# Performance work log

Measured on AMD Instinct MI355X. Metric: run time of the kernel, lower is better.

The kernel has to match this reference:

```python
import jax, jax.numpy as jnp
import numpy as np

B, S, I, E, NH, HID, L = 32, 512, 64, 128, 8, 1024, 4
HD = E // NH
TEMP = 0.05
EPS_BN = 1e-5
EPS_LN = 1e-5


def _pe(seq_len, d_model):
    # sinusoidal positional encoding, matches PositionalEncoding buffer pe[:seq_len, 0, :]
    pos = jnp.arange(seq_len, dtype=jnp.float32)[:, None]
    div = jnp.exp(jnp.arange(0, d_model, 2, dtype=jnp.float32) * (-np.log(10000.0) / d_model))
    pe = jnp.zeros((seq_len, d_model), jnp.float32)
    pe = pe.at[:, 0::2].set(jnp.sin(pos * div))
    pe = pe.at[:, 1::2].set(jnp.cos(pos * div))
    return pe


def _bn(x, g, b, axis):
    # eval-mode BatchNorm1d with running_mean=0, running_var=1 (affine scale+shift)
    sh = [1] * x.ndim
    sh[axis] = -1
    return x * (g / jnp.sqrt(1.0 + EPS_BN)).reshape(sh) + b.reshape(sh)


def _ln(x, g, b):
    m = jnp.mean(x, axis=-1, keepdims=True)
    v = jnp.var(x, axis=-1, keepdims=True)
    return (x - m) / jnp.sqrt(v + EPS_LN) * g + b


def _layer(h, Wqkv, bqkv, Wo, bo, g1, b1, g2, b2, W1, bf1, W2, bf2):
    # h: (S, B, E); post-LN torch TransformerEncoderLayer, relu FFN
    s, b = h.shape[0], h.shape[1]
    qkv = h @ Wqkv + bqkv                                  # (S, B, 3E)
    q, k, v = jnp.split(qkv, 3, axis=-1)
    sp = lambda t: t.reshape(s, b, NH, HD).transpose(1, 2, 0, 3)  # (B, NH, S, HD)
    q, k, v = sp(q), sp(k), sp(v)
    att = jax.nn.softmax(jnp.einsum('bhqd,bhkd->bhqk', q, k) * (1.0 / np.sqrt(HD)), axis=-1)
    o = jnp.einsum('bhqk,bhkd->bhqd', att, v).transpose(2, 0, 1, 3).reshape(s, b, E)
    h = _ln(h + o @ Wo + bo, g1, b1)
    ff = jax.nn.relu(h @ W1 + bf1) @ W2 + bf2
    h = _ln(h + ff, g2, b2)
    return h, att.mean(axis=1)  # attn averaged over heads: (B, S, S)


def setup_inputs() -> dict:
    key = jax.random.key(0)
    ks = iter(jax.random.split(key, 64))
    r = lambda *sh: jax.random.normal(next(ks), sh, jnp.float32) * 0.02
    return dict(
        x=jax.random.normal(next(ks), (B, S, I), jnp.float32),
        Wt=r(I, E), bt=r(E),
        bn1_g=jnp.ones(E), bn1_b=jnp.zeros(E),
        bn2_g=jnp.ones(E), bn2_b=jnp.zeros(E),
        Wqkv=r(L, E, 3 * E), bqkv=r(L, 3 * E), Wo=r(L, E, E), bo=r(L, E),
        ln1_g=jnp.ones((L, E)), ln1_b=jnp.zeros((L, E)),
        ln2_g=jnp.ones((L, E)), ln2_b=jnp.zeros((L, E)),
        W1=r(L, E, HID), b1=r(L, HID), W2=r(L, HID, E), b2=r(L, E),
        bn3_g=jnp.ones(E), bn3_b=jnp.zeros(E),
        Wd=r(E, I), bd=r(I), bn4_g=jnp.ones(I), bn4_b=jnp.zeros(I),
        Ws=r(S, HID), bs=r(HID), bn5_g=jnp.ones(HID), bn5_b=jnp.zeros(HID),
        Wtext=r(1024, HID), btext=r(HID), lnT_g=jnp.ones(HID), lnT_b=jnp.zeros(HID),
        sensor_emb=jax.random.normal(next(ks), (I, 1024), jnp.float32),
    )


def reference(x, Wt, bt, bn1_g, bn1_b, bn2_g, bn2_b,
              Wqkv, bqkv, Wo, bo, ln1_g, ln1_b, ln2_g, ln2_b,
              W1, b1, W2, b2, bn3_g, bn3_b,
              Wd, bd, bn4_g, bn4_b, Ws, bs, bn5_g, bn5_b,
              Wtext, btext, lnT_g, lnT_b, sensor_emb):
    # trunk_net: Linear -> BN(E) -> PE -> BN(E)
    h = x @ Wt + bt                                  # (B, S, E)
    h = _bn(h.transpose(0, 2, 1), bn1_g, bn1_b, 1)   # (B, E, S)
    h = h.transpose(2, 0, 1)                         # (S, B, E)
    h = h + _pe(h.shape[0], E)[:, None, :]
    h = _bn(h.transpose(1, 2, 0), bn2_g, bn2_b, 1)   # (B, E, S)
    h = h.transpose(2, 0, 1)                         # (S, B, E)
    for i in range(L):
        h, attn = _layer(h, Wqkv[i], bqkv[i], Wo[i], bo[i],
                         ln1_g[i], ln1_b[i], ln2_g[i], ln2_b[i],
                         W1[i], b1[i], W2[i], b2[i])
    h = _bn(h.transpose(1, 2, 0), bn3_g, bn3_b, 1)   # (B, E, S)
    # downsample_embedding_to_input_net
    d = jax.nn.relu(h.transpose(0, 2, 1) @ Wd + bd)  # (B, S, I)
    d = _bn(d.transpose(0, 2, 1), bn4_g, bn4_b, 1)   # (B, I, S)
    # sequence_representation_net
    imu = jax.nn.relu(d @ Ws + bs)                   # (B, I, HID)
    imu = _bn(imu, bn5_g, bn5_b, 2)
    # text_to_shared_net on sensor embeddings
    sens = _ln(jax.nn.relu(sensor_emb @ Wtext + btext), lnT_g, lnT_b)  # (I, HID)
    # fused pairwise cosine similarity (torch expands to (B,I,I,HID); we don't)
    imu_n = imu / jnp.maximum(jnp.linalg.norm(imu, axis=-1, keepdims=True), 1e-8)
    sens_n = sens / jnp.maximum(jnp.linalg.norm(sens, axis=-1, keepdims=True), 1e-8)
    return jnp.einsum('bih,jh->bij', imu_n, sens_n) / TEMP  # (B, I, I)
```

## Files before the change

### kernel.cpp

```cpp
#include <hip/hip_runtime.h>
#include <hip/hip_bf16.h>

#define B_   32
#define S_   512
#define I_   64
#define E_   128
#define NH_  8
#define HD_  16
#define HID_ 1024
#define L_   4
#define NTOK (B_*S_)

typedef __hip_bfloat16 bf16;
typedef __attribute__((ext_vector_type(8))) short bf16x8;
typedef __attribute__((ext_vector_type(4))) short bf16x4;
typedef __attribute__((ext_vector_type(4))) float f32x4;

__device__ __forceinline__ float b2f(bf16 v) { return __bfloat162float(v); }

template<bool F32>
__device__ __forceinline__ float ld(const void* p, size_t i) {
    if (F32) return ((const float*)p)[i];
    return b2f(((const bf16*)p)[i]);
}

__device__ __forceinline__ unsigned short f2bu(float f) {
    union { bf16 h; unsigned short u; } c; c.h = __float2bfloat16(f); return c.u;
}
__device__ __forceinline__ unsigned short b2u(bf16 h) {
    union { bf16 h; unsigned short u; } c; c.h = h; return c.u;
}
__device__ __forceinline__ float u2f(unsigned short u) {
    return __uint_as_float((unsigned int)u << 16);
}

__global__ void k_flag(const void* bn1g, int* flag) {
    if (threadIdx.x == 0) {
        const unsigned short* u = (const unsigned short*)bn1g;
        int zeros = 0;
        for (int i = 0; i < 32; ++i) zeros += (u[i] == 0);
        flag[0] = (zeros >= 8) ? 1 : 0;
    }
}

struct TrJobs {
    const void* in[7];
    bf16*       out[7];
    int R[7];
    int C[7];
    int start[8];
};

template<bool F32>
__device__ void tr_all_body(const TrJobs& j, float (*tile)[33])
{
    int bid = blockIdx.x;
    int job = 0;
#pragma unroll
    for (int t = 0; t < 6; ++t) if (bid >= j.start[t + 1]) job = t + 1;
    int local = bid - j.start[job];
    int R = j.R[job], C = j.C[job];
    int nx = C >> 5, ny = R >> 5;
    int per_z = nx * ny;
    int z = local / per_z;
    int rem = local - z * per_z;
    int cy = rem / nx, cx = rem - cy * nx;
    const void* in = j.in[job];
    bf16* out = j.out[job];

    size_t off = (size_t)z * R * C;
    int c0 = cx * 32, r0 = cy * 32;
    int tx = threadIdx.x;
    for (int i = threadIdx.y; i < 32; i += 8)
        tile[i][tx] = ld<F32>(in, off + (size_t)(r0 + i) * C + c0 + tx);
    __syncthreads();
    for (int i = threadIdx.y; i < 32; i += 8)
        out[off + (size_t)(c0 + i) * R + r0 + tx] = __float2bfloat16(tile[tx][i]);
}
__global__ __launch_bounds__(256) void k_tr_all(TrJobs j, const int* flag)
{
    __shared__ float tile[32][33];
    if (*flag) tr_all_body<true>(j, tile);
    else       tr_all_body<false>(j, tile);
}

template<bool F32>
__device__ void trunk_body(const void* x, const void* Wt, const void* bt,
                           const void* g1, const void* c1,
                           const void* g2, const void* c2, float* __restrict__ h,
                           float (*xs)[I_])
{
    const int TOK = 8;
    int t0 = blockIdx.x * TOK;
    int tid = threadIdx.x;
    for (int idx = tid; idx < TOK * I_; idx += 128) {
        int tt = idx >> 6, k = idx & 63;
        xs[tt][k] = ld<F32>(x, (size_t)(t0 + tt) * I_ + k);
    }
    __syncthreads();
    int e = tid;
    float acc[TOK];
    float bias = ld<F32>(bt, e);
#pragma unroll
    for (int tt = 0; tt < TOK; ++tt) acc[tt] = bias;
    for (int k = 0; k < I_; ++k) {
        float w = ld<F32>(Wt, k * E_ + e);
#pragma unroll
        for (int tt = 0; tt < TOK; ++tt) acc[tt] += xs[tt][k] * w;
    }
    float rs = rsqrtf(1.0f + 1e-5f);
    float a1 = ld<F32>(g1, e) * rs, d1 = ld<F32>(c1, e);
    float a2 = ld<F32>(g2, e) * rs, d2 = ld<F32>(c2, e);
    int p = e >> 1;
    float freq = __expf(-(float)p * 0.14391157f);
#pragma unroll
    for (int tt = 0; tt < TOK; ++tt) {
// ... 84 lines not shown
    const size_t base = (size_t)(b * S_) * 384 + hh * HD_;
    const float qs = 0.25f * 1.44269504f;

    for (int i = tid; i < S_ * 2; i += 512) {
        int s = i >> 1, hf = i & 1;
        uint4 v = *(const uint4*)(qkv + base + (size_t)s * 384 + 128 + hf * 8);
        unsigned int* w = (unsigned int*)&v;
#pragma unroll
        for (int j = 0; j < 4; ++j) {
            unsigned int lo = f2bu(u2f((unsigned short)(w[j] & 0xffff)) * qs);
            unsigned int hi = f2bu(u2f((unsigned short)(w[j] >> 16)) * qs);
            w[j] = lo | (hi << 16);
        }
        *(uint4*)&Ks[s * 16 + hf * 8] = v;
    }
    for (int i = tid; i < 256 * 2; i += 512) {
        int s = i >> 1, hf = i & 1;
        *(uint4*)&Qs[s * 16 + hf * 8] =
            *(const uint4*)(qkv + base + (size_t)(qh * 256 + s) * 384 + hf * 8);
    }
    {
        int s = tid;
        uint4 v0 = *(const uint4*)(qkv + base + (size_t)s * 384 + 256);
        uint4 v1 = *(const uint4*)(qkv + base + (size_t)s * 384 + 256 + 8);
        const unsigned short* u0 = (const unsigned short*)&v0;
        const unsigned short* u1 = (const unsigned short*)&v1;
#pragma unroll
        for (int dd = 0; dd < 8; ++dd) VT[dd * 520 + s] = u0[dd];
#pragma unroll
        for (int dd = 0; dd < 8; ++dd) VT[(8 + dd) * 520 + s] = u1[dd];
    }
    __syncthreads();

    int wv = tid >> 6, lane = tid & 63;
    int l15 = lane & 15, quad = lane >> 4;
    const f32x4 z4 = {0.f, 0.f, 0.f, 0.f};

    bf16x4 bq0 = *(const bf16x4*)&Qs[(wv * 32 + l15) * 16 + quad * 4];
    bf16x4 bq1 = *(const bf16x4*)&Qs[(wv * 32 + 16 + l15) * 16 + quad * 4];

    f32x4 O0 = z4, O1 = z4;
    float den0 = 0.f, den1 = 0.f;

#pragma unroll 2
    for (int kt = 0; kt < 32; ++kt) {
        bf16x4 ak = *(const bf16x4*)&Ks[(kt * 16 + l15) * 16 + quad * 4];
        bf16x4 av = *(const bf16x4*)&VT[l15 * 520 + kt * 16 + quad * 4];

        f32x4 s0 = __builtin_amdgcn_mfma_f32_16x16x16bf16_1k(ak, bq0, z4, 0, 0, 0);
        f32x4 s1 = __builtin_amdgcn_mfma_f32_16x16x16bf16_1k(ak, bq1, z4, 0, 0, 0);

        float p0[4], p1[4];
#pragma unroll
        for (int r = 0; r < 4; ++r) { p0[r] = exp2f(s0[r]); den0 += p0[r]; }
#pragma unroll
        for (int r = 0; r < 4; ++r) { p1[r] = exp2f(s1[r]); den1 += p1[r]; }

        bf16x4 pa0, pa1;
#pragma unroll
        for (int r = 0; r < 4; ++r) { pa0[r] = (short)f2bu(p0[r]); pa1[r] = (short)f2bu(p1[r]); }

        O0 = __builtin_amdgcn_mfma_f32_16x16x16bf16_1k(av, pa0, O0, 0, 0, 0);
        O1 = __builtin_amdgcn_mfma_f32_16x16x16bf16_1k(av, pa1, O1, 0, 0, 0);
    }

    den0 += __shfl_xor(den0, 16, 64);
    den0 += __shfl_xor(den0, 32, 64);
    den1 += __shfl_xor(den1, 16, 64);
    den1 += __shfl_xor(den1, 32, 64);
    float inv0 = 1.0f / den0;
    float inv1 = 1.0f / den1;

    int q0 = qh * 256 + wv * 32 + l15;
    bf16* out0 = qkv + (size_t)(b * S_ + q0) * 384 + hh * HD_ + quad * 4;
    bf16* out1 = out0 + (size_t)16 * 384;
    unsigned int a0 = (unsigned int)f2bu(O0[0] * inv0) | ((unsigned int)f2bu(O0[1] * inv0) << 16);
    unsigned int a1 = (unsigned int)f2bu(O0[2] * inv0) | ((unsigned int)f2bu(O0[3] * inv0) << 16);
    *(uint2*)out0 = (uint2){a0, a1};
    unsigned int c0 = (unsigned int)f2bu(O1[0] * inv1) | ((unsigned int)f2bu(O1[1] * inv1) << 16);
    unsigned int c1 = (unsigned int)f2bu(O1[2] * inv1) | ((unsigned int)f2bu(O1[3] * inv1) << 16);
    *(uint2*)out1 = (uint2){c0, c1};
}

#define FTOK 32
#define APAD 8
#define MPAD 8

template<bool F32>
__device__ void projffn_body(const bf16* __restrict__ qkv, const bf16* __restrict__ WoT,
                             const void* bo, size_t obo,
                             const void* g1, const void* be1,
                             const bf16* __restrict__ W1T, const void* b1, size_t ob1,
                             const bf16* __restrict__ W2T, const void* b2v, size_t ob2,
                             const void* g2, const void* be2, size_t oln,
                             float* __restrict__ h,
                             unsigned short (*A_s)[E_ + APAD],
                             unsigned short (*mid_s)[HID_ + MPAD],
                             float (*red)[32][2])
{
    int t0 = blockIdx.x * FTOK;
    int tid = threadIdx.x;
    int wv = tid >> 6, lane = tid & 63;
    int l15 = lane & 15, quad = lane >> 4;
    int c0 = wv * 32 + l15, c1 = c0 + 16;

    for (int i = tid; i < 32 * 16; i += 256) {
        int row = i >> 4, seg = i & 15;
        *(uint4*)&A_s[row][seg * 8] =
            *(const uint4*)&qkv[(size_t)(t0 + row) * 384 + seg * 8];
    }
    __syncthreads();

    bf16x8 af[2][4];
#pragma unroll
    for (int kt = 0; kt < 4; ++kt) {
        int k0 = kt * 32 + quad * 8;
        af[0][kt] = *(const bf16x8*)&A_s[l15][k0];
        af[1][kt] = *(const bf16x8*)&A_s[16 + l15][k0];
    }
    f32x4 acc[2][2];
#pragma unroll
    for (int a = 0; a < 2; ++a)
#pragma unroll
        for (int bn = 0; bn < 2; ++bn) acc[a][bn] = (f32x4){0.f, 0.f, 0.f, 0.f};
#pragma unroll
    for (int kt = 0; kt < 4; ++kt) {
        int k0 = kt * 32 + quad * 8;
        bf16x8 bb0 = *(const bf16x8*)&WoT[(size_t)c0 * E_ + k0];
        bf16x8 bb1 = *(const bf16x8*)&WoT[(size_t)c1 * E_ + k0];
        acc[0][0] = __builtin_amdgcn_mfma_f32_16x16x32_bf16(af[0][kt], bb0, acc[0][0], 0, 0, 0);
        acc[1][0] = __builtin_amdgcn_mfma_f32_16x16x32_bf16(af[1][kt], bb0, acc[1][0], 0, 0, 0);
        acc[0][1] = __builtin_amdgcn_mfma_f32_16x16x32_bf16(af[0][kt], bb1, acc[0][1], 0, 0, 0);
        acc[1][1] = __builtin_amdgcn_mfma_f32_16x16x32_bf16(af[1][kt], bb1, acc[1][1], 0, 0, 0);
    }

    float bo0 = ld<F32>(bo, obo + c0), bo1 = ld<F32>(bo, obo + c1);
    float val[2][2][4], s1[2][4], s2[2][4];
#pragma unroll
    for (int mt = 0; mt < 2; ++mt) {
#pragma unroll
        for (int r = 0; r < 4; ++r) {
            size_t row = (size_t)(t0 + mt * 16 + quad * 4 + r);
            float v0 = acc[mt][0][r] + bo0 + h[row * E_ + c0];
            float v1 = acc[mt][1][r] + bo1 + h[row * E_ + c1];
            val[mt][0][r] = v0; val[mt][1][r] = v1;
            s1[mt][r] = v0 + v1;
            s2[mt][r] = v0 * v0 + v1 * v1;
        }
    }
#pragma unroll
    for (int off = 1; off < 16; off <<= 1) {
#pragma unroll
        for (int mt = 0; mt < 2; ++mt)
#pragma unroll
            for (int r = 0; r < 4; ++r) {
                s1[mt][r] += __shfl_xor(s1[mt][r], off, 64);
                s2[mt][r] += __shfl_xor(s2[mt][r], off, 64);
            }
    }
    if (l15 == 0) {
#pragma unroll
        for (int mt = 0; mt < 2; ++mt)
#pragma unroll
            for (int r = 0; r < 4; ++r) {
                red[wv][mt * 16 + quad * 4 + r][0] = s1[mt][r];
                red[wv][mt * 16 + quad * 4 + r][1] = s2[mt][r];
            }
    }
    __syncthreads();

    float val1[2][2][4];
    {
        float g10 = ld<F32>(g1, oln + c0), g11 = ld<F32>(g1, oln + c1);
        float b10 = ld<F32>(be1, oln + c0), b11 = ld<F32>(be1, oln + c1);
#pragma unroll
        for (int mt = 0; mt < 2; ++mt) {
#pragma unroll
            for (int r = 0; r < 4; ++r) {
                int rw = mt * 16 + quad * 4 + r;
                float su = red[0][rw][0] + red[1][rw][0] + red[2][rw][0] + red[3][rw][0];
                float sq = red[0][rw][1] + red[1][rw][1] + red[2][rw][1] + red[3][rw][1];
                float mean = su * (1.0f / E_);
                float var = fmaxf(sq * (1.0f / E_) - mean * mean, 0.0f);
                float rstd = rsqrtf(var + 1e-5f);
                float h0 = (val[mt][0][r] - mean) * rstd * g10 + b10;
                float h1v = (val[mt][1][r] - mean) * rstd * g11 + b11;
                val1[mt][0][r] = h0; val1[mt][1][r] = h1v;
                A_s[rw][c0] = f2bu(h0);
                A_s[rw][c1] = f2bu(h1v);
            }
        }
    }
    __syncthreads();

    {
        bf16x8 af1[2][4];
#pragma unroll
        for (int kt = 0; kt < 4; ++kt) {
            int k0 = kt * 32 + quad * 8;
            af1[0][kt] = *(const bf16x8*)&A_s[l15][k0];
            af1[1][kt] = *(const bf16x8*)&A_s[16 + l15][k0];
        }
        for (int nt = 0; nt < 16; ++nt) {
            int col = wv * 256 + nt * 16 + l15;
            f32x4 acc0 = {0.f, 0.f, 0.f, 0.f}, acc1 = {0.f, 0.f, 0.f, 0.f};
#pragma unroll
            for (int kt = 0; kt < 4; ++kt) {
                bf16x8 bfr = *(const bf16x8*)&W1T[(size_t)col * E_ + kt * 32 + quad * 8];
                acc0 = __builtin_amdgcn_mfma_f32_16x16x32_bf16(af1[0][kt], bfr, acc0, 0, 0, 0);
                acc1 = __builtin_amdgcn_mfma_f32_16x16x32_bf16(af1[1][kt], bfr, acc1, 0, 0, 0);
            }
            float bias = ld<F32>(b1, ob1 + col);
#pragma unroll
            for (int r = 0; r < 4; ++r) {
                mid_s[quad * 4 + r][col]      = f2bu(fmaxf(acc0[r] + bias, 0.f));
                mid_s[16 + quad * 4 + r][col] = f2bu(fmaxf(acc1[r] + bias, 0.f));
            }
        }
    }
    __syncthreads();

    f32x4 acc2[2][2];
#pragma unroll
    for (int a = 0; a < 2; ++a)
#pragma unroll
        for (int bn = 0; bn < 2; ++bn) acc2[a][bn] = (f32x4){0.f, 0.f, 0.f, 0.f};
    for (int kt = 0; kt < 32; ++kt) {
        int k0 = kt * 32 + quad * 8;
        bf16x8 a0 = *(const bf16x8*)&mid_s[l15][k0];
        bf16x8 a1 = *(const bf16x8*)&mid_s[16 + l15][k0];
        bf16x8 bb0 = *(const bf16x8*)&W2T[(size_t)c0 * HID_ + k0];
        bf16x8 bb1 = *(const bf16x8*)&W2T[(size_t)c1 * HID_ + k0];
        acc2[0][0] = __builtin_amdgcn_mfma_f32_16x16x32_bf16(a0, bb0, acc2[0][0], 0, 0, 0);
        acc2[1][0] = __builtin_amdgcn_mfma_f32_16x16x32_bf16(a1, bb0, acc2[1][0], 0, 0, 0);
        acc2[0][1] = __builtin_amdgcn_mfma_f32_16x16x32_bf16(a0, bb1, acc2[0][1], 0, 0, 0);
        acc2[1][1] = __builtin_amdgcn_mfma_f32_16x16x32_bf16(a1, bb1, acc2[1][1], 0, 0, 0);
    }

    float b20 = ld<F32>(b2v, ob2 + c0), b21 = ld<F32>(b2v, ob2 + c1);
#pragma unroll
    for (int mt = 0; mt < 2; ++mt) {
#pragma unroll
        for (int r = 0; r < 4; ++r) {
            float v0 = acc2[mt][0][r] + b20 + val1[mt][0][r];
            float v1 = acc2[mt][1][r] + b21 + val1[mt][1][r];
            val[mt][0][r] = v0; val[mt][1][r] = v1;
            s1[mt][r] = v0 + v1;
            s2[mt][r] = v0 * v0 + v1 * v1;
        }
    }
#pragma unroll
    for (int off = 1; off < 16; off <<= 1) {
#pragma unroll
        for (int mt = 0; mt < 2; ++mt)
#pragma unroll
            for (int r = 0; r < 4; ++r) {
                s1[mt][r] += __shfl_xor(s1[mt][r], off, 64);
                s2[mt][r] += __shfl_xor(s2[mt][r], off, 64);
            }
    }
    if (l15 == 0) {
#pragma unroll
        for (int mt = 0; mt < 2; ++mt)
#pragma unroll
            for (int r = 0; r < 4; ++r) {
                red[wv][mt * 16 + quad * 4 + r][0] = s1[mt][r];
                red[wv][mt * 16 + quad * 4 + r][1] = s2[mt][r];
            }
    }
    __syncthreads();
    float g20 = ld<F32>(g2, oln + c0), g21 = ld<F32>(g2, oln + c1);
    float be20 = ld<F32>(be2, oln + c0), be21 = ld<F32>(be2, oln + c1);
#pragma unroll
    for (int mt = 0; mt < 2; ++mt) {
#pragma unroll
        for (int r = 0; r < 4; ++r) {
            int rw = mt * 16 + quad * 4 + r;
            float su = red[0][rw][0] + red[1][rw][0] + red[2][rw][0] + red[3][rw][0];
            float sq = red[0][rw][1] + red[1][rw][1] + red[2][rw][1] + red[3][rw][1];
            float mean = su * (1.0f / E_);
            float var = fmaxf(sq * (1.0f / E_) - mean * mean, 0.0f);
            float rstd = rsqrtf(var + 1e-5f);
            size_t row = (size_t)(t0 + rw);
            h[row * E_ + c0] = (val[mt][0][r] - mean) * rstd * g20 + be20;
            h[row * E_ + c1] = (val[mt][1][r] - mean) * rstd * g21 + be21;
        }
    }
}
__global__ __launch_bounds__(256) void k_projffn(
    const bf16* qkv, const bf16* WoT, const void* bo, size_t obo,
    const void* g1, const void* be1,
    const bf16* W1T, const void* b1, size_t ob1,
    const bf16* W2T, const void* b2v, size_t ob2,
    const void* g2, const void* be2, size_t oln, float* h, const int* flag)
{
    __shared__ unsigned short A_s[FTOK][E_ + APAD];
    __shared__ unsigned short mid_s[FTOK][HID_ + MPAD];
    __shared__ float red[4][32][2];
    if (*flag) projffn_body<true>(qkv, WoT, bo, obo, g1, be1, W1T, b1, ob1,
                                  W2T, b2v, ob2, g2, be2, oln, h, A_s, mid_s, red);
    else       projffn_body<false>(qkv, WoT, bo, obo, g1, be1, W1T, b1, ob1,
                                   W2T, b2v, ob2, g2, be2, oln, h, A_s, mid_s, red);
}

template<bool F32>
__device__ void downm_body(const float* __restrict__ h, const void* g3, const void* c3,
                           const bf16* __restrict__ WdT, const void* bd,
                           const void* g4, const void* c4, float* __restrict__ d,
                           unsigned short (*A_s)[136], float* g3s, float* c3s)
{
    int t0 = blockIdx.x * 32;
    int tid = threadIdx.x;
    if (tid < E_) {
        float rs = rsqrtf(1.0f + 1e-5f);
        g3s[tid] = ld<F32>(g3, tid) * rs;
        c3s[tid] = ld<F32>(c3, tid);
    }
    __syncthreads();
    for (int i = tid; i < 32 * E_; i += 256) {
        int row = i >> 7, col = i & 127;
        A_s[row][col] = f2bu(h[(size_t)(t0 + row) * E_ + col] * g3s[col] + c3s[col]);
    }
    __syncthreads();

    int wv = tid >> 6, lane = tid & 63;
    int l15 = lane & 15, quad = lane >> 4;
    int col = wv * 16 + l15;
    f32x4 acc0 = {0.f, 0.f, 0.f, 0.f}, acc1 = {0.f, 0.f, 0.f, 0.f};
#pragma unroll
    for (int kt = 0; kt < 4; ++kt) {
        int k0 = kt * 32 + quad * 8;
        bf16x8 a0 = *(const bf16x8*)&A_s[l15][k0];
        bf16x8 a1 = *(const bf16x8*)&A_s[16 + l15][k0];
        bf16x8 bb = *(const bf16x8*)&WdT[(size_t)col * E_ + k0];
        acc0 = __builtin_amdgcn_mfma_f32_16x16x32_bf16(a0, bb, acc0, 0, 0, 0);
        acc1 = __builtin_amdgcn_mfma_f32_16x16x32_bf16(a1, bb, acc1, 0, 0, 0);
    }
    float rs = rsqrtf(1.0f + 1e-5f);
    float bb = ld<F32>(bd, col);
    float a4 = ld<F32>(g4, col) * rs, d4 = ld<F32>(c4, col);
#pragma unroll
    for (int r = 0; r < 4; ++r) {
        d[(size_t)(t0 + quad * 4 + r) * I_ + col]      = fmaxf(acc0[r] + bb, 0.f) * a4 + d4;
        d[(size_t)(t0 + 16 + quad * 4 + r) * I_ + col] = fmaxf(acc1[r] + bb, 0.f) * a4 + d4;
    }
}
__global__ __launch_bounds__(256) void k_down(
    const float* h, const void* g3, const void* c3, const bf16* WdT, const void* bd,
    const void* g4, const void* c4, float* d, const int* flag)
{
    __shared__ unsigned short A_s[32][136];
    __shared__ float g3s[E_], c3s[E_];
    if (*flag) downm_body<true>(h, g3, c3, WdT, bd, g4, c4, d, A_s, g3s, c3s);
    else       downm_body<false>(h, g3, c3, WdT, bd, g4, c4, d, A_s, g3s, c3s);
}

template<bool F32>
__device__ void imum_body(const float* __restrict__ d, const bf16* __restrict__ WsT,
                          const void* bs, const void* g5, const void* c5,
                          float* __restrict__ imu, unsigned short (*A_s)[520])
{
    int b = blockIdx.x >> 3;
    int jc = blockIdx.x & 7;
    int tid = threadIdx.x;
    int wv = tid >> 6, lane = tid & 63;
    int l15 = lane & 15, quad = lane >> 4;

    for (int idx = tid; idx < I_ * S_; idx += 256) {
        int i = idx & 63, s = idx >> 6;
        A_s[i][s] = f2bu(d[((size_t)b * S_ + s) * I_ + i]);
    }
    __syncthreads();

    float rs = rsqrtf(1.0f + 1e-5f);
    int j0 = jc * 128 + wv * 32;
    for (int nt = 0; nt < 2; ++nt) {
        int j = j0 + nt * 16 + l15;
        f32x4 acc4[4];
#pragma unroll
        for (int mt = 0; mt < 4; ++mt) acc4[mt] = (f32x4){0.f, 0.f, 0.f, 0.f};
        for (int kt = 0; kt < 16; ++kt) {
            int k0 = kt * 32 + quad * 8;
            bf16x8 bfr = *(const bf16x8*)&WsT[(size_t)j * S_ + k0];
#pragma unroll
            for (int mt = 0; mt < 4; ++mt) {
// ... 184 lines not shown
extern "C" void kernel_launch(void* const* d_in, const int* in_sizes, int n_in,
                              void* d_out, int out_size, void* d_ws, size_t ws_size,
                              hipStream_t stream) {
    (void)in_sizes; (void)n_in; (void)out_size; (void)ws_size;
    const void* x      = d_in[0];
    const void* Wt     = d_in[1];
    const void* bt     = d_in[2];
    const void* bn1_g  = d_in[3];
    const void* bn1_b  = d_in[4];
    const void* bn2_g  = d_in[5];
    const void* bn2_b  = d_in[6];
    const void* Wqkv   = d_in[7];
    const void* bqkv   = d_in[8];
    const void* Wo     = d_in[9];
    const void* bo     = d_in[10];
    const void* ln1_g  = d_in[11];
    const void* ln1_b  = d_in[12];
    const void* ln2_g  = d_in[13];
    const void* ln2_b  = d_in[14];
    const void* W1     = d_in[15];
    const void* b1     = d_in[16];
    const void* W2     = d_in[17];
    const void* b2     = d_in[18];
    const void* bn3_g  = d_in[19];
    const void* bn3_b  = d_in[20];
    const void* Wd     = d_in[21];
    const void* bd     = d_in[22];
    const void* bn4_g  = d_in[23];
    const void* bn4_b  = d_in[24];
    const void* Wsr    = d_in[25];
    const void* bs     = d_in[26];
    const void* bn5_g  = d_in[27];
    const void* bn5_b  = d_in[28];
    const void* Wtext  = d_in[29];
    const void* btext  = d_in[30];
    const void* lnT_g  = d_in[31];
    const void* lnT_b  = d_in[32];
    const void* semb   = d_in[33];

    char* ws = (char*)d_ws;
    float* h    = (float*)(ws);
    bf16*  qkvb = (bf16*) (ws + ((size_t)8  << 20));
    float* dbuf = (float*)(ws + ((size_t)8  << 20));
    float* imu  = (float*)(ws + ((size_t)12 << 20));
    bf16*  wb   = (bf16*) (ws + ((size_t)20 << 20));
    bf16*  WqkvT = wb;
    bf16*  WoT   = wb + 196608;
    bf16*  W1T   = wb + 262144;
    bf16*  W2T   = wb + 786432;
    bf16*  WsT   = wb + 1310720;
    bf16*  sensb = wb + 1835008;
    bf16*  WdT   = wb + 1900544;
    float* sg    = (float*)(wb + 1908736);
    int*   flag  = (int*)  (ws + ((size_t)24 << 20));
    bf16*  WtxT  = (bf16*) (ws + ((size_t)25 << 20));

    k_flag<<<1, 64, 0, stream>>>(bn1_g, flag);

    {
        TrJobs tj;
        tj.in[0] = Wqkv;  tj.out[0] = WqkvT; tj.R[0] = 128;  tj.C[0] = 384;
        tj.in[1] = Wo;    tj.out[1] = WoT;   tj.R[1] = 128;  tj.C[1] = 128;
        tj.in[2] = W1;    tj.out[2] = W1T;   tj.R[2] = 128;  tj.C[2] = 1024;
        tj.in[3] = W2;    tj.out[3] = W2T;   tj.R[3] = 1024; tj.C[3] = 128;
        tj.in[4] = Wsr;   tj.out[4] = WsT;   tj.R[4] = 512;  tj.C[4] = 1024;
        tj.in[5] = Wd;    tj.out[5] = WdT;   tj.R[5] = 128;  tj.C[5] = 64;
        tj.in[6] = Wtext; tj.out[6] = WtxT;  tj.R[6] = 1024; tj.C[6] = 1024;
        const int st[8] = {0, 192, 256, 768, 1280, 1792, 1800, 2824};
        for (int i = 0; i < 8; ++i) tj.start[i] = st[i];
        k_tr_all<<<2824, dim3(32, 8), 0, stream>>>(tj, flag);
    }

    k_trunk<<<NTOK / 8, 128, 0, stream>>>(x, Wt, bt, bn1_g, bn1_b, bn2_g, bn2_b, h, flag);

    for (int l = 0; l < L_; ++l) {
        size_t obqkv = (size_t)l * 384;
        size_t obo   = (size_t)l * E_;
        size_t ob1   = (size_t)l * HID_;
        size_t ob2   = (size_t)l * E_;
        size_t oln   = (size_t)l * E_;
        k_qkv<<<NTOK / 32, 256, 0, stream>>>(h, WqkvT + (size_t)l * 49152,
                                             bqkv, obqkv, qkvb, flag);
        k_attn<<<B_ * NH_ * 2, 512, 0, stream>>>(qkvb);
        k_projffn<<<NTOK / 32, 256, 0, stream>>>(qkvb, WoT + (size_t)l * 16384, bo, obo,
                                                 ln1_g, ln1_b,
                                                 W1T + (size_t)l * 131072, b1, ob1,
                                                 W2T + (size_t)l * 131072, b2, ob2,
                                                 ln2_g, ln2_b, oln, h, flag);
    }

    k_down<<<NTOK / 32, 256, 0, stream>>>(h, bn3_g, bn3_b, WdT, bd, bn4_g, bn4_b, dbuf, flag);
    k_imu<<<B_ * 8, 256, 0, stream>>>(dbuf, WsT, bs, bn5_g, bn5_b, imu, flag);
    k_norm<<<B_ * I_, 256, 0, stream>>>(imu);
    k_sens_gemm<<<64, 256, 0, stream>>>(semb, WtxT, btext, sg, flag);
    k_sens_ln<<<I_, 256, 0, stream>>>(sg, lnT_g, lnT_b, sensb, flag);
    k_final<<<(B_ * I_) / 32, 256, 0, stream>>>(imu, sensb, d_out, flag);
}
```

Baseline: 520.8 us.

## Restructure fused proj+FFN kernel to register-resident per-wave token tiles without LDS

Rewrites the output-projection + LayerNorm + FFN + LayerNorm kernel so each wave owns 16 tokens and computes transposed MFMAs (weights as A operand, tokens as B) with 16x16x16 bf16 instructions. Activations stay in registers across the chain, so the LDS staging buffers, the cross-wave reductions and the block barriers go away, and the FFN hidden activation is consumed immediately per 16-column chunk instead of being written to a 32x1024 shared buffer. Grid halves to 64 tokens per block. The trade-off is more weight traffic per token from global/L2, since each wave reloads all weights, plus heavier register pressure.

```diff
diff --git a/kernel.cpp b/kernel.cpp
--- a/kernel.cpp
+++ b/kernel.cpp
@@ -32,6 +32,14 @@
 }
 __device__ __forceinline__ float u2f(unsigned short u) {
     return __uint_as_float((unsigned int)u << 16);
+}
+
+template<bool F32>
+__device__ __forceinline__ float4 ld4(const void* p, size_t i) {
+    if (F32) return *(const float4*)((const float*)p + i);
+    bf16x4 v = *(const bf16x4*)((const bf16*)p + i);
+    return make_float4(u2f((unsigned short)v[0]), u2f((unsigned short)v[1]),
+                       u2f((unsigned short)v[2]), u2f((unsigned short)v[3]));
 }
 
 __global__ void k_flag(const void* bn1g, int* flag) {
@@ -282,9 +290,7 @@
     *(uint2*)out1 = (uint2){c0, c1};
 }
 
-#define FTOK 32
-#define APAD 8
-#define MPAD 8
+#define MFMA16(A, Bv, C) __builtin_amdgcn_mfma_f32_16x16x16bf16_1k(A, Bv, C, 0, 0, 0)
 
 template<bool F32>
 __device__ void projffn_body(const bf16* __restrict__ qkv, const bf16* __restrict__ WoT,
@@ -293,197 +299,125 @@
                              const bf16* __restrict__ W1T, const void* b1, size_t ob1,
                              const bf16* __restrict__ W2T, const void* b2v, size_t ob2,
                              const void* g2, const void* be2, size_t oln,
-                             float* __restrict__ h,
-                             unsigned short (*A_s)[E_ + APAD],
-                             unsigned short (*mid_s)[HID_ + MPAD],
-                             float (*red)[32][2])
-{
-    int t0 = blockIdx.x * FTOK;
-    int tid = threadIdx.x;
-    int wv = tid >> 6, lane = tid & 63;
+                             float* __restrict__ h)
+{
+    int wv = threadIdx.x >> 6, lane = threadIdx.x & 63;
     int l15 = lane & 15, quad = lane >> 4;
-    int c0 = wv * 32 + l15, c1 = c0 + 16;
-
-    for (int i = tid; i < 32 * 16; i += 256) {
-        int row = i >> 4, seg = i & 15;
-        *(uint4*)&A_s[row][seg * 8] =
-            *(const uint4*)&qkv[(size_t)(t0 + row) * 384 + seg * 8];
-    }
-    __syncthreads();
-
-    bf16x8 af[2][4];
-#pragma unroll
-    for (int kt = 0; kt < 4; ++kt) {
-        int k0 = kt * 32 + quad * 8;
-        af[0][kt] = *(const bf16x8*)&A_s[l15][k0];
-        af[1][kt] = *(const bf16x8*)&A_s[16 + l15][k0];
-    }
-    f32x4 acc[2][2];
-#pragma unroll
-    for (int a = 0; a < 2; ++a)
-#pragma unroll
-        for (int bn = 0; bn < 2; ++bn) acc[a][bn] = (f32x4){0.f, 0.f, 0.f, 0.f};
-#pragma unroll
-    for (int kt = 0; kt < 4; ++kt) {
-        int k0 = kt * 32 + quad * 8;
-        bf16x8 bb0 = *(const bf16x8*)&WoT[(size_t)c0 * E_ + k0];
-        bf16x8 bb1 = *(const bf16x8*)&WoT[(size_t)c1 * E_ + k0];
-        acc[0][0] = __builtin_amdgcn_mfma_f32_16x16x32_bf16(af[0][kt], bb0, acc[0][0], 0, 0, 0);
-        acc[1][0] = __builtin_amdgcn_mfma_f32_16x16x32_bf16(af[1][kt], bb0, acc[1][0], 0, 0, 0);
-        acc[0][1] = __builtin_amdgcn_mfma_f32_16x16x32_bf16(af[0][kt], bb1, acc[0][1], 0, 0, 0);
-        acc[1][1] = __builtin_amdgcn_mfma_f32_16x16x32_bf16(af[1][kt], bb1, acc[1][1], 0, 0, 0);
-    }
-
-    float bo0 = ld<F32>(bo, obo + c0), bo1 = ld<F32>(bo, obo + c1);
-    float val[2][2][4], s1[2][4], s2[2][4];
-#pragma unroll
-    for (int mt = 0; mt < 2; ++mt) {
-#pragma unroll
-        for (int r = 0; r < 4; ++r) {
-            size_t row = (size_t)(t0 + mt * 16 + quad * 4 + r);
-            float v0 = acc[mt][0][r] + bo0 + h[row * E_ + c0];
-            float v1 = acc[mt][1][r] + bo1 + h[row * E_ + c1];
-            val[mt][0][r] = v0; val[mt][1][r] = v1;
-            s1[mt][r] = v0 + v1;
-            s2[mt][r] = v0 * v0 + v1 * v1;
-        }
-    }
-#pragma unroll
-    for (int off = 1; off < 16; off <<= 1) {
-#pragma unroll
-        for (int mt = 0; mt < 2; ++mt)
-#pragma unroll
-            for (int r = 0; r < 4; ++r) {
-                s1[mt][r] += __shfl_xor(s1[mt][r], off, 64);
-                s2[mt][r] += __shfl_xor(s2[mt][r], off, 64);
-            }
-    }
-    if (l15 == 0) {
-#pragma unroll
-        for (int mt = 0; mt < 2; ++mt)
-#pragma unroll
-            for (int r = 0; r < 4; ++r) {
-                red[wv][mt * 16 + quad * 4 + r][0] = s1[mt][r];
-                red[wv][mt * 16 + quad * 4 + r][1] = s2[mt][r];
-            }
-    }
-    __syncthreads();
-
-    float val1[2][2][4];
+    int tok = blockIdx.x * 64 + wv * 16 + l15;
+    const f32x4 z4 = {0.f, 0.f, 0.f, 0.f};
+    int cq = quad * 4;
+
+    bf16x4 ofr[8];
+#pragma unroll
+    for (int kt = 0; kt < 8; ++kt)
+        ofr[kt] = *(const bf16x4*)&qkv[(size_t)tok * 384 + kt * 16 + cq];
+
+    f32x4 v1[8];
+#pragma unroll
+    for (int ot = 0; ot < 8; ++ot) {
+        f32x4 ca = z4, cb = z4;
+        const bf16* wrow = &WoT[(size_t)(ot * 16 + l15) * E_ + cq];
+#pragma unroll
+        for (int kt = 0; kt < 4; ++kt) {
+            bf16x4 a0 = *(const bf16x4*)&wrow[kt * 16];
+            bf16x4 a1 = *(const bf16x4*)&wrow[(kt + 4) * 16];
+            ca = MFMA16(a0, ofr[kt], ca);
+            cb = MFMA16(a1, ofr[kt + 4], cb);
+        }
+        float4 hres = *(const float4*)&h[(size_t)tok * E_ + ot * 16 + cq];
+        float4 bb = ld4<F32>(bo, obo + ot * 16 + cq);
+        v1[ot][0] = ca[0] + cb[0] + bb.x + hres.x;
+        v1[ot][1] = ca[1] + cb[1] + bb.y + hres.y;
+        v1[ot][2] = ca[2] + cb[2] + bb.z + hres.z;
+        v1[ot][3] = ca[3] + cb[3] + bb.w + hres.w;
+    }
+
     {
-        float g10 = ld<F32>(g1, oln + c0), g11 = ld<F32>(g1, oln + c1);
-        float b10 = ld<F32>(be1, oln + c0), b11 = ld<F32>(be1, oln + c1);
-#pragma unroll
-        for (int mt = 0; mt < 2; ++mt) {
-#pragma unroll
-            for (int r = 0; r < 4; ++r) {
-                int rw = mt * 16 + quad * 4 + r;
-                float su = red[0][rw][0] + red[1][rw][0] + red[2][rw][0] + red[3][rw][0];
-                float sq = red[0][rw][1] + red[1][rw][1] + red[2][rw][1] + red[3][rw][1];
-                float mean = su * (1.0f / E_);
-                float var = fmaxf(sq * (1.0f / E_) - mean * mean, 0.0f);
-                float rstd = rsqrtf(var + 1e-5f);
-                float h0 = (val[mt][0][r] - mean) * rstd * g10 + b10;
-                float h1v = (val[mt][1][r] - mean) * rstd * g11 + b11;
-                val1[mt][0][r] = h0; val1[mt][1][r] = h1v;
-                A_s[rw][c0] = f2bu(h0);
-                A_s[rw][c1] = f2bu(h1v);
-            }
-        }
-    }
-    __syncthreads();
+        float s1 = 0.f, s2 = 0.f;
+#pragma unroll
+        for (int ot = 0; ot < 8; ++ot)
+#pragma unroll
+            for (int r = 0; r < 4; ++r) { float v = v1[ot][r]; s1 += v; s2 += v * v; }
+        s1 += __shfl_xor(s1, 16, 64); s1 += __shfl_xor(s1, 32, 64);
+        s2 += __shfl_xor(s2, 16, 64); s2 += __shfl_xor(s2, 32, 64);
+        float mean = s1 * (1.0f / E_);
+        float var = fmaxf(s2 * (1.0f / E_) - mean * mean, 0.0f);
+        float rstd = rsqrtf(var + 1e-5f);
+#pragma unroll
+        for (int ot = 0; ot < 8; ++ot) {
+            float4 gg = ld4<F32>(g1, oln + ot * 16 + cq);
+            float4 be = ld4<F32>(be1, oln + ot * 16 + cq);
+            v1[ot][0] = (v1[ot][0] - mean) * rstd * gg.x + be.x;
+            v1[ot][1] = (v1[ot][1] - mean) * rstd * gg.y + be.y;
+            v1[ot][2] = (v1[ot][2] - mean) * rstd * gg.z + be.z;
+            v1[ot][3] = (v1[ot][3] - mean) * rstd * gg.w + be.w;
+        }
+    }
+
+    bf16x4 h1f[8];
+#pragma unroll
+    for (int ot = 0; ot < 8; ++ot) {
+        h1f[ot][0] = (short)f2bu(v1[ot][0]);
+        h1f[ot][1] = (short)f2bu(v1[ot][1]);
+        h1f[ot][2] = (short)f2bu(v1[ot][2]);
+        h1f[ot][3] = (short)f2bu(v1[ot][3]);
+    }
+
+    f32x4 o2[8];
+#pragma unroll
+    for (int ot = 0; ot < 8; ++ot) o2[ot] = z4;
+
+#pragma unroll 2
+    for (int mt = 0; mt < 64; ++mt) {
+        f32x4 c1a = z4, c1b = z4;
+        const bf16* w1row = &W1T[(size_t)(mt * 16 + l15) * E_ + cq];
+#pragma unroll
+        for (int kt = 0; kt < 4; ++kt) {
+            bf16x4 a0 = *(const bf16x4*)&w1row[kt * 16];
+            bf16x4 a1 = *(const bf16x4*)&w1row[(kt + 4) * 16];
+            c1a = MFMA16(a0, h1f[kt], c1a);
+            c1b = MFMA16(a1, h1f[kt + 4], c1b);
+        }
+        float4 b1v = ld4<F32>(b1, ob1 + mt * 16 + cq);
+        bf16x4 mf;
+        mf[0] = (short)f2bu(fmaxf(c1a[0] + c1b[0] + b1v.x, 0.f));
+        mf[1] = (short)f2bu(fmaxf(c1a[1] + c1b[1] + b1v.y, 0.f));
+        mf[2] = (short)f2bu(fmaxf(c1a[2] + c1b[2] + b1v.z, 0.f));
+        mf[3] = (short)f2bu(fmaxf(c1a[3] + c1b[3] + b1v.w, 0.f));
+#pragma unroll
+        for (int ot = 0; ot < 8; ++ot) {
+            bf16x4 a = *(const bf16x4*)&W2T[(size_t)(ot * 16 + l15) * HID_ + mt * 16 + cq];
+            o2[ot] = MFMA16(a, mf, o2[ot]);
+        }
+    }
 
     {
-        bf16x8 af1[2][4];
-#pragma unroll
-        for (int kt = 0; kt < 4; ++kt) {
-            int k0 = kt * 32 + quad * 8;
-            af1[0][kt] = *(const bf16x8*)&A_s[l15][k0];
-            af1[1][kt] = *(const bf16x8*)&A_s[16 + l15][k0];
-        }
-        for (int nt = 0; nt < 16; ++nt) {
-            int col = wv * 256 + nt * 16 + l15;
-            f32x4 acc0 = {0.f, 0.f, 0.f, 0.f}, acc1 = {0.f, 0.f, 0.f, 0.f};
-#pragma unroll
-            for (int kt = 0; kt < 4; ++kt) {
-                bf16x8 bfr = *(const bf16x8*)&W1T[(size_t)col * E_ + kt * 32 + quad * 8];
-                acc0 = __builtin_amdgcn_mfma_f32_16x16x32_bf16(af1[0][kt], bfr, acc0, 0, 0, 0);
-                acc1 = __builtin_amdgcn_mfma_f32_16x16x32_bf16(af1[1][kt], bfr, acc1, 0, 0, 0);
-            }
-            float bias = ld<F32>(b1, ob1 + col);
-#pragma unroll
-            for (int r = 0; r < 4; ++r) {
-                mid_s[quad * 4 + r][col]      = f2bu(fmaxf(acc0[r] + bias, 0.f));
-                mid_s[16 + quad * 4 + r][col] = f2bu(fmaxf(acc1[r] + bias, 0.f));
-            }
-        }
-    }
-    __syncthreads();
-
-    f32x4 acc2[2][2];
-#pragma unroll
-    for (int a = 0; a < 2; ++a)
-#pragma unroll
-        for (int bn = 0; bn < 2; ++bn) acc2[a][bn] = (f32x4){0.f, 0.f, 0.f, 0.f};
-    for (int kt = 0; kt < 32; ++kt) {
-        int k0 = kt * 32 + quad * 8;
-        bf16x8 a0 = *(const bf16x8*)&mid_s[l15][k0];
-        bf16x8 a1 = *(const bf16x8*)&mid_s[16 + l15][k0];
-        bf16x8 bb0 = *(const bf16x8*)&W2T[(size_t)c0 * HID_ + k0];
-        bf16x8 bb1 = *(const bf16x8*)&W2T[(size_t)c1 * HID_ + k0];
-        acc2[0][0] = __builtin_amdgcn_mfma_f32_16x16x32_bf16(a0, bb0, acc2[0][0], 0, 0, 0);
-        acc2[1][0] = __builtin_amdgcn_mfma_f32_16x16x32_bf16(a1, bb0, acc2[1][0], 0, 0, 0);
-        acc2[0][1] = __builtin_amdgcn_mfma_f32_16x16x32_bf16(a0, bb1, acc2[0][1], 0, 0, 0);
-        acc2[1][1] = __builtin_amdgcn_mfma_f32_16x16x32_bf16(a1, bb1, acc2[1][1], 0, 0, 0);
-    }
-
-    float b20 = ld<F32>(b2v, ob2 + c0), b21 = ld<F32>(b2v, ob2 + c1);
-#pragma unroll
-    for (int mt = 0; mt < 2; ++mt) {
-#pragma unroll
-        for (int r = 0; r < 4; ++r) {
-            float v0 = acc2[mt][0][r] + b20 + val1[mt][0][r];
-            float v1 = acc2[mt][1][r] + b21 + val1[mt][1][r];
-            val[mt][0][r] = v0; val[mt][1][r] = v1;
-            s1[mt][r] = v0 + v1;
-            s2[mt][r] = v0 * v0 + v1 * v1;
-        }
-    }
-#pragma unroll
-    for (int off = 1; off < 16; off <<= 1) {
-#pragma unroll
-        for (int mt = 0; mt < 2; ++mt)
-#pragma unroll
-            for (int r = 0; r < 4; ++r) {
-                s1[mt][r] += __shfl_xor(s1[mt][r], off, 64);
-                s2[mt][r] += __shfl_xor(s2[mt][r], off, 64);
-            }
-    }
-    if (l15 == 0) {
-#pragma unroll
-        for (int mt = 0; mt < 2; ++mt)
-#pragma unroll
-            for (int r = 0; r < 4; ++r) {
-                red[wv][mt * 16 + quad * 4 + r][0] = s1[mt][r];
-                red[wv][mt * 16 + quad * 4 + r][1] = s2[mt][r];
-            }
-    }
-    __syncthreads();
-    float g20 = ld<F32>(g2, oln + c0), g21 = ld<F32>(g2, oln + c1);
-    float be20 = ld<F32>(be2, oln + c0), be21 = ld<F32>(be2, oln + c1);
-#pragma unroll
-    for (int mt = 0; mt < 2; ++mt) {
-#pragma unroll
-        for (int r = 0; r < 4; ++r) {
-            int rw = mt * 16 + quad * 4 + r;
-            float su = red[0][rw][0] + red[1][rw][0] + red[2][rw][0] + red[3][rw][0];
-            float sq = red[0][rw][1] + red[1][rw][1] + red[2][rw][1] + red[3][rw][1];
-            float mean = su * (1.0f / E_);
-            float var = fmaxf(sq * (1.0f / E_) - mean * mean, 0.0f);
-            float rstd = rsqrtf(var + 1e-5f);
-            size_t row = (size_t)(t0 + rw);
-            h[row * E_ + c0] = (val[mt][0][r] - mean) * rstd * g20 + be20;
-            h[row * E_ + c1] = (val[mt][1][r] - mean) * rstd * g21 + be21;
+        float s1 = 0.f, s2 = 0.f;
+#pragma unroll
+        for (int ot = 0; ot < 8; ++ot) {
+            float4 bb = ld4<F32>(b2v, ob2 + ot * 16 + cq);
+            o2[ot][0] += bb.x + v1[ot][0];
+            o2[ot][1] += bb.y + v1[ot][1];
+            o2[ot][2] += bb.z + v1[ot][2];
+            o2[ot][3] += bb.w + v1[ot][3];
+#pragma unroll
+            for (int r = 0; r < 4; ++r) { float v = o2[ot][r]; s1 += v; s2 += v * v; }
+        }
+        s1 += __shfl_xor(s1, 16, 64); s1 += __shfl_xor(s1, 32, 64);
+        s2 += __shfl_xor(s2, 16, 64); s2 += __shfl_xor(s2, 32, 64);
+        float mean = s1 * (1.0f / E_);
+        float var = fmaxf(s2 * (1.0f / E_) - mean * mean, 0.0f);
+        float rstd = rsqrtf(var + 1e-5f);
+#pragma unroll
+        for (int ot = 0; ot < 8; ++ot) {
+            float4 gg = ld4<F32>(g2, oln + ot * 16 + cq);
+            float4 be = ld4<F32>(be2, oln + ot * 16 + cq);
+            float4 outv;
+            outv.x = (o2[ot][0] - mean) * rstd * gg.x + be.x;
+            outv.y = (o2[ot][1] - mean) * rstd * gg.y + be.y;
+            outv.z = (o2[ot][2] - mean) * rstd * gg.z + be.z;
+            outv.w = (o2[ot][3] - mean) * rstd * gg.w + be.w;
+            *(float4*)&h[(size_t)tok * E_ + ot * 16 + cq] = outv;
         }
     }
 }
@@ -494,13 +428,10 @@
     const bf16* W2T, const void* b2v, size_t ob2,
     const void* g2, const void* be2, size_t oln, float* h, const int* flag)
 {
-    __shared__ unsigned short A_s[FTOK][E_ + APAD];
-    __shared__ unsigned short mid_s[FTOK][HID_ + MPAD];
-    __shared__ float red[4][32][2];
     if (*flag) projffn_body<true>(qkv, WoT, bo, obo, g1, be1, W1T, b1, ob1,
-                                  W2T, b2v, ob2, g2, be2, oln, h, A_s, mid_s, red);
+                                  W2T, b2v, ob2, g2, be2, oln, h);
     else       projffn_body<false>(qkv, WoT, bo, obo, g1, be1, W1T, b1, ob1,
-                                   W2T, b2v, ob2, g2, be2, oln, h, A_s, mid_s, red);
+                                   W2T, b2v, ob2, g2, be2, oln, h);
 }
 
 template<bool F32>
@@ -851,7 +782,7 @@
         k_qkv<<<NTOK / 32, 256, 0, stream>>>(h, WqkvT + (size_t)l * 49152,
                                              bqkv, obqkv, qkvb, flag);
         k_attn<<<B_ * NH_ * 2, 512, 0, stream>>>(qkvb);
-        k_projffn<<<NTOK / 32, 256, 0, stream>>>(qkvb, WoT + (size_t)l * 16384, bo, obo,
+        k_projffn<<<NTOK / 64, 256, 0, stream>>>(qkvb, WoT + (size_t)l * 16384, bo, obo,
                                                  ln1_g, ln1_b,
                                                  W1T + (size_t)l * 131072, b1, ob1,
                                                  W2T + (size_t)l * 131072, b2, ob2,
```

New measurement: 876.8 us. +68.3%, slower.

## Split FFN hidden dimension into two halves to shrink shared memory in projffn

Applied to the files above, without the earlier changes.

The FFN in the fused proj+FFN kernel now processes the 1024-wide hidden layer in two 512-wide passes. Each pass computes half of the ReLU activations into a smaller shared buffer, then accumulates that half into the W2 output. This roughly halves the mid_s LDS footprint, and launch bounds now request 3 blocks per CU so more blocks can be resident. In exchange it adds extra barriers per block and may constrain registers.

```diff
diff --git a/kernel.cpp b/kernel.cpp
--- a/kernel.cpp
+++ b/kernel.cpp
@@ -284,6 +284,7 @@
 
 #define FTOK 32
 #define APAD 8
+#define MHALF 512
 #define MPAD 8
 
 template<bool F32>
@@ -295,7 +296,7 @@
                              const void* g2, const void* be2, size_t oln,
                              float* __restrict__ h,
                              unsigned short (*A_s)[E_ + APAD],
-                             unsigned short (*mid_s)[HID_ + MPAD],
+                             unsigned short (*mid_s)[MHALF + MPAD],
                              float (*red)[32][2])
 {
     int t0 = blockIdx.x * FTOK;
@@ -393,16 +394,24 @@
     }
     __syncthreads();
 
-    {
-        bf16x8 af1[2][4];
-#pragma unroll
-        for (int kt = 0; kt < 4; ++kt) {
-            int k0 = kt * 32 + quad * 8;
-            af1[0][kt] = *(const bf16x8*)&A_s[l15][k0];
-            af1[1][kt] = *(const bf16x8*)&A_s[16 + l15][k0];
-        }
-        for (int nt = 0; nt < 16; ++nt) {
-            int col = wv * 256 + nt * 16 + l15;
+    bf16x8 af1[2][4];
+#pragma unroll
+    for (int kt = 0; kt < 4; ++kt) {
+        int k0 = kt * 32 + quad * 8;
+        af1[0][kt] = *(const bf16x8*)&A_s[l15][k0];
+        af1[1][kt] = *(const bf16x8*)&A_s[16 + l15][k0];
+    }
+
+    f32x4 acc2[2][2];
+#pragma unroll
+    for (int a = 0; a < 2; ++a)
+#pragma unroll
+        for (int bn = 0; bn < 2; ++bn) acc2[a][bn] = (f32x4){0.f, 0.f, 0.f, 0.f};
+
+    for (int p = 0; p < 2; ++p) {
+        for (int nt = 0; nt < 8; ++nt) {
+            int col = p * MHALF + wv * 128 + nt * 16 + l15;
+            int lc  = wv * 128 + nt * 16 + l15;
             f32x4 acc0 = {0.f, 0.f, 0.f, 0.f}, acc1 = {0.f, 0.f, 0.f, 0.f};
 #pragma unroll
             for (int kt = 0; kt < 4; ++kt) {
@@ -413,28 +422,26 @@
             float bias = ld<F32>(b1, ob1 + col);
 #pragma unroll
             for (int r = 0; r < 4; ++r) {
-                mid_s[quad * 4 + r][col]      = f2bu(fmaxf(acc0[r] + bias, 0.f));
-                mid_s[16 + quad * 4 + r][col] = f2bu(fmaxf(acc1[r] + bias, 0.f));
+                mid_s[quad * 4 + r][lc]      = f2bu(fmaxf(acc0[r] + bias, 0.f));
+                mid_s[16 + quad * 4 + r][lc] = f2bu(fmaxf(acc1[r] + bias, 0.f));
             }
         }
-    }
-    __syncthreads();
-
-    f32x4 acc2[2][2];
-#pragma unroll
-    for (int a = 0; a < 2; ++a)
-#pragma unroll
-        for (int bn = 0; bn < 2; ++bn) acc2[a][bn] = (f32x4){0.f, 0.f, 0.f, 0.f};
-    for (int kt = 0; kt < 32; ++kt) {
-        int k0 = kt * 32 + quad * 8;
-        bf16x8 a0 = *(const bf16x8*)&mid_s[l15][k0];
-        bf16x8 a1 = *(const bf16x8*)&mid_s[16 + l15][k0];
-        bf16x8 bb0 = *(const bf16x8*)&W2T[(size_t)c0 * HID_ + k0];
-        bf16x8 bb1 = *(const bf16x8*)&W2T[(size_t)c1 * HID_ + k0];
-        acc2[0][0] = __builtin_amdgcn_mfma_f32_16x16x32_bf16(a0, bb0, acc2[0][0], 0, 0, 0);
-        acc2[1][0] = __builtin_amdgcn_mfma_f32_16x16x32_bf16(a1, bb0, acc2[1][0], 0, 0, 0);
-        acc2[0][1] = __builtin_amdgcn_mfma_f32_16x16x32_bf16(a0, bb1, acc2[0][1], 0, 0, 0);
-        acc2[1][1] = __builtin_amdgcn_mfma_f32_16x16x32_bf16(a1, bb1, acc2[1][1], 0, 0, 0);
+        __syncthreads();
+
+        for (int kk = 0; kk < 16; ++kk) {
+            int kt = p * 16 + kk;
+            int k0l = kk * 32 + quad * 8;
+            int k0g = kt * 32 + quad * 8;
+            bf16x8 a0 = *(const bf16x8*)&mid_s[l15][k0l];
+            bf16x8 a1 = *(const bf16x8*)&mid_s[16 + l15][k0l];
+            bf16x8 bb0 = *(const bf16x8*)&W2T[(size_t)c0 * HID_ + k0g];
+            bf16x8 bb1 = *(const bf16x8*)&W2T[(size_t)c1 * HID_ + k0g];
+            acc2[0][0] = __builtin_amdgcn_mfma_f32_16x16x32_bf16(a0, bb0, acc2[0][0], 0, 0, 0);
+            acc2[1][0] = __builtin_amdgcn_mfma_f32_16x16x32_bf16(a1, bb0, acc2[1][0], 0, 0, 0);
+            acc2[0][1] = __builtin_amdgcn_mfma_f32_16x16x32_bf16(a0, bb1, acc2[0][1], 0, 0, 0);
+            acc2[1][1] = __builtin_amdgcn_mfma_f32_16x16x32_bf16(a1, bb1, acc2[1][1], 0, 0, 0);
+        }
+        __syncthreads();
     }
 
     float b20 = ld<F32>(b2v, ob2 + c0), b21 = ld<F32>(b2v, ob2 + c1);
@@ -487,7 +494,7 @@
         }
     }
 }
-__global__ __launch_bounds__(256) void k_projffn(
+__global__ __launch_bounds__(256, 3) void k_projffn(
     const bf16* qkv, const bf16* WoT, const void* bo, size_t obo,
     const void* g1, const void* be1,
     const bf16* W1T, const void* b1, size_t ob1,
@@ -495,7 +502,7 @@
     const void* g2, const void* be2, size_t oln, float* h, const int* flag)
 {
     __shared__ unsigned short A_s[FTOK][E_ + APAD];
-    __shared__ unsigned short mid_s[FTOK][HID_ + MPAD];
+    __shared__ unsigned short mid_s[FTOK][MHALF + MPAD];
     __shared__ float red[4][32][2];
     if (*flag) projffn_body<true>(qkv, WoT, bo, obo, g1, be1, W1T, b1, ob1,
                                   W2T, b2v, ob2, g2, be2, oln, h, A_s, mid_s, red);
@@ -851,11 +858,11 @@
         k_qkv<<<NTOK / 32, 256, 0, stream>>>(h, WqkvT + (size_t)l * 49152,
                                              bqkv, obqkv, qkvb, flag);
         k_attn<<<B_ * NH_ * 2, 512, 0, stream>>>(qkvb);
-        k_projffn<<<NTOK / 32, 256, 0, stream>>>(qkvb, WoT + (size_t)l * 16384, bo, obo,
-                                                 ln1_g, ln1_b,
-                                                 W1T + (size_t)l * 131072, b1, ob1,
-                                                 W2T + (size_t)l * 131072, b2, ob2,
-                                                 ln2_g, ln2_b, oln, h, flag);
+        k_projffn<<<NTOK / FTOK, 256, 0, stream>>>(qkvb, WoT + (size_t)l * 16384, bo, obo,
+                                                   ln1_g, ln1_b,
+                                                   W1T + (size_t)l * 131072, b1, ob1,
+                                                   W2T + (size_t)l * 131072, b2, ob2,
+                                                   ln2_g, ln2_b, oln, h, flag);
     }
 
     k_down<<<NTOK / 32, 256, 0, stream>>>(h, bn3_g, bn3_b, WdT, bd, bn4_g, bn4_b, dbuf, flag);
```

After: 542.1 us. +4.1%, slower.
